# Optimization experiments

Hardware: AMD Instinct MI355X
Metric: run time of the kernel (lower is better)

Reference implementation:

```python
import jax, jax.numpy as jnp
import numpy as np

WS = 8          # window_size
DISP = WS // 2  # cyclic shift displacement
HEADS = 12
HEAD_DIM = 32
SCALE = HEAD_DIM ** -0.5


def _rel_indices():
    # indices of (x, y) for x in range(WS) for y in range(WS)
    idx = np.stack(np.meshgrid(np.arange(WS), np.arange(WS), indexing='ij'), -1).reshape(-1, 2)
    return idx[None, :, :] - idx[:, None, :] + WS - 1  # (WS^2, WS^2, 2), values in [0, 2*WS-2]


def _masks():
    ninf = -np.inf
    # upper/lower mask: blocks attention across the vertical wrap boundary
    m_ul = np.zeros((WS * WS, WS * WS), np.float32)
    m_ul[-DISP * WS:, :-DISP * WS] = ninf
    m_ul[:-DISP * WS, -DISP * WS:] = ninf
    # left/right mask: blocks attention across the horizontal wrap boundary
    m4 = np.zeros((WS, WS, WS, WS), np.float32)  # (h1, w1, h2, w2)
    m4[:, -DISP:, :, :-DISP] = ninf
    m4[:, :-DISP, :, -DISP:] = ninf
    m_lr = m4.reshape(WS * WS, WS * WS)
    return jnp.asarray(m_ul), jnp.asarray(m_lr)


def setup_inputs() -> dict:
    key = jax.random.key(0)
    k1, k2, k3, k4, k5 = jax.random.split(key, 5)
    dim = HEADS * HEAD_DIM  # 384
    return {
        'x': jax.random.normal(k1, (16, 64, 64, dim), jnp.float32),
        'w_qkv': jax.random.normal(k2, (dim, 3 * dim), jnp.float32) * 0.02,
        'pos_embedding': jax.random.normal(k3, (2 * WS - 1, 2 * WS - 1), jnp.float32),
        'w_out': jax.random.normal(k4, (dim, dim), jnp.float32) * 0.02,
        'b_out': jax.random.normal(k5, (dim,), jnp.float32) * 0.02,
    }


def reference(x, w_qkv, pos_embedding, w_out, b_out):
    b, H, W, dim = x.shape
    nw_h, nw_w = H // WS, W // WS
    # cyclic shift
    x = jnp.roll(x, (-DISP, -DISP), axis=(1, 2))
    qkv = x @ w_qkv  # (b, H, W, 3*inner)

    def to_windows(t):
        # (b, H, W, inner) -> (b, heads, nw_h*nw_w, WS*WS, head_dim)
        t = t.reshape(b, nw_h, WS, nw_w, WS, HEADS, HEAD_DIM)
        return t.transpose(0, 5, 1, 3, 2, 4, 6).reshape(b, HEADS, nw_h * nw_w, WS * WS, HEAD_DIM)

    q, k, v = [to_windows(t) for t in jnp.split(qkv, 3, axis=-1)]
    dots = jnp.einsum('bhwid,bhwjd->bhwij', q, k) * SCALE

    rel = _rel_indices()
    dots = dots + pos_embedding[rel[..., 0], rel[..., 1]]  # relative position bias

    m_ul, m_lr = _masks()
    dots = dots.at[:, :, -nw_w:].add(m_ul)            # last row of windows
    dots = dots.at[:, :, nw_w - 1::nw_w].add(m_lr)    # last column of windows

    attn = jax.nn.softmax(dots, axis=-1)
    out = jnp.einsum('bhwij,bhwjd->bhwid', attn, v)
    # windows -> image layout
    out = out.reshape(b, HEADS, nw_h, nw_w, WS, WS, HEAD_DIM)
    out = out.transpose(0, 2, 4, 3, 5, 1, 6).reshape(b, H, W, HEADS * HEAD_DIM)
    out = out @ w_out + b_out
    # cyclic back shift
    return jnp.roll(out, (DISP, DISP), axis=(1, 2))
```

## Files before the change

### kernel.cpp

```cpp
#include <hip/hip_runtime.h>
#include <stdint.h>

#define HEADS 12
#define HD 32
#define DIM 384
#define NQKV 1152
#define NPIX 4096
#define NB 16

typedef __attribute__((ext_vector_type(8))) short bf16x8;
typedef __attribute__((ext_vector_type(4))) float f32x4;

__device__ __forceinline__ unsigned short f2bf(float f) {
  uint32_t u = __builtin_bit_cast(uint32_t, f);
  u += 0x7FFF + ((u >> 16) & 1);
  return (unsigned short)(u >> 16);
}

__device__ __forceinline__ uint32_t cvtpk(float lo, float hi) {
  uint32_t r;
  asm("v_cvt_pk_bf16_f32 %0, %1, %2" : "=v"(r) : "v"(lo), "v"(hi));
  return r;
}

#define GL_LDS(gp, lp) __builtin_amdgcn_global_load_lds( \
    (const __attribute__((address_space(1))) void*)(gp),  \
    (__attribute__((address_space(3))) void*)(lp), 16, 0, 0)

#define MFMA32 __builtin_amdgcn_mfma_f32_16x16x32_bf16

__global__ void convert_w(const float* __restrict__ wqkv,
                          const float* __restrict__ wout,
                          const float* __restrict__ pos,
                          unsigned short* __restrict__ wqkvT,
                          unsigned short* __restrict__ woutT,
                          float* __restrict__ tab) {
  int bid = blockIdx.x;
  if (bid < 1728) {
    int tid = bid * 256 + threadIdx.x;
    if (tid < NQKV * DIM) {
      int n = tid / DIM, k = tid % DIM;
      wqkvT[tid] = f2bf(wqkv[(size_t)k * NQKV + n]);
    }
    if (tid < DIM * DIM) {
      int n = tid / DIM, k = tid % DIM;
      woutT[tid] = f2bf(wout[(size_t)k * DIM + n]);
    }
  } else {
    int tid = (bid - 1728) * 256 + threadIdx.x;
    int v = tid >> 12, rem = tid & 4095;
    int i = rem >> 6, j = rem & 63;
    int xi = i >> 3, yi = i & 7, xj = j >> 3, yj = j & 7;
    float val = pos[(xj - xi + 7) * 15 + (yj - yi + 7)];
    if ((v & 1) && ((i >= 32) != (j >= 32))) val = -1e30f;
    if ((v & 2) && ((yi >= 4) != (yj >= 4))) val = -1e30f;
    tab[tid] = val;
  }
}

__global__ __launch_bounds__(256, 3) void gemm_qkv(
    const float* __restrict__ x,
    const unsigned short* __restrict__ wT,
    unsigned short* __restrict__ qkv)
{
  __shared__ float lAf[128 * 64];
  __shared__ unsigned short lB[128 * 64];
  const int tid = threadIdx.x;
  const int wid = tid >> 6, lane = tid & 63;
  const int wr = wid >> 1, wc = wid & 1;
  const int lr = lane >> 4, lc = lane & 15;

  const int f = blockIdx.x;
  const int xcd = f & 7, idx = f >> 3;
  const int nt = idx % 9, mt = xcd * 64 + idx / 9;
  const int m0 = mt * 128, n0 = nt * 128;

  const int sArow = wid * 4 + (lane >> 4);
  const int sAcol = ((lane & 15) ^ sArow) * 4;
  const float* agp = x + (size_t)(m0 + sArow) * DIM + sAcol;

  const int sBrow = wid * 32 + (lane >> 3);
  const int sBcol = ((lane & 7) ^ (lane >> 3)) * 8;
  const unsigned short* bgp = wT + (size_t)(n0 + sBrow) * DIM + sBcol;

  const f32x4 z4 = {0.f, 0.f, 0.f, 0.f};
  f32x4 acc[4][4];
#pragma unroll
  for (int i = 0; i < 4; i++)
#pragma unroll
    for (int j = 0; j < 4; j++) acc[i][j] = z4;

  auto stage = [&](int t) {
#pragma unroll
    for (int i = 0; i < 8; i++)
      GL_LDS(agp + (size_t)(i * 16) * DIM + t * 64, &lAf[i * 1024 + wid * 256]);
#pragma unroll
    for (int i = 0; i < 4; i++)
      GL_LDS(bgp + (size_t)(i * 8) * DIM + t * 64, &lB[(wid * 4 + i) * 512]);
  };
  auto compute = [&]() {
    const int swb = lc & 7;
#pragma unroll
    for (int kk = 0; kk < 2; kk++) {
      bf16x8 afr[4], bfr[4];
#pragma unroll
      for (int mi = 0; mi < 4; mi++) {
        const int r = wr * 64 + mi * 16 + lc;
        const int g0 = kk * 8 + lr * 2;
        float4 a0 = *(const float4*)&lAf[r * 64 + ((g0 ^ lc) * 4)];
        float4 a1 = *(const float4*)&lAf[r * 64 + (((g0 + 1) ^ lc) * 4)];
        union { uint32_t u[4]; bf16x8 v; } up;
        up.u[0] = cvtpk(a0.x, a0.y);
        up.u[1] = cvtpk(a0.z, a0.w);
        up.u[2] = cvtpk(a1.x, a1.y);
        up.u[3] = cvtpk(a1.z, a1.w);
        afr[mi] = up.v;
      }
#pragma unroll
      for (int ni = 0; ni < 4; ni++)
        bfr[ni] = *(const bf16x8*)&lB[(wc * 64 + ni * 16 + lc) * 64 + (((kk * 4 + lr) ^ swb) * 8)];
#pragma unroll
      for (int mi = 0; mi < 4; mi++)
#pragma unroll
        for (int ni = 0; ni < 4; ni++)
          acc[mi][ni] = MFMA32(afr[mi], bfr[ni], acc[mi][ni], 0, 0, 0);
    }
  };

  for (int t = 0; t < 6; ++t) {
    stage(t);
    __syncthreads();
    compute();
    if (t < 5) __syncthreads();
  }

#pragma unroll
  for (int mi = 0; mi < 4; mi++) {
    int row = m0 + wr * 64 + mi * 16 + lr * 4;
#pragma unroll
    for (int reg = 0; reg < 4; reg++) {
      size_t rb = (size_t)(row + reg) * NQKV + n0 + wc * 64 + lc;
#pragma unroll
      for (int ni = 0; ni < 4; ni++)
        qkv[rb + ni * 16] = f2bf(acc[mi][ni][reg]);
    }
  }
}

__global__ __launch_bounds__(256) void attn_kernel(
    const unsigned short* __restrict__ qkv,
    const float* __restrict__ tab,
    unsigned short* __restrict__ Z)
{
  __shared__ unsigned short Vt[4][32 * 80];

  const int wid = threadIdx.x >> 6, lane = threadIdx.x & 63;
  const int lr = lane >> 4, lc = lane & 15;
  const int task = blockIdx.x * 4 + wid;
  const int win = task & 63;
  const int head = (task >> 6) % HEADS;
  const int b = task / (HEADS * 64);
  const int wh = win >> 3, ww = win & 7;
  const float* tv = tab + (((wh == 7) ? 1 : 0) + ((ww == 7) ? 2 : 0)) * 4096;

  auto pixof = [&](int t) {
    int hh = (wh * 8 + (t >> 3) + 4) & 63;
    int w2 = (ww * 8 + (t & 7) + 4) & 63;
    return hh * 64 + w2;
  };

  unsigned short* vt = &Vt[wid][0];
  bf16x8 qf[4], kf[4];
#pragma unroll
  for (int g = 0; g < 4; ++g) {
    int t = g * 16 + lc;
    const unsigned short* base =
        qkv + (size_t)(b * NPIX + pixof(t)) * NQKV + head * HD + lr * 8;
    qf[g] = *(const bf16x8*)(base);
    kf[g] = *(const bf16x8*)(base + DIM);
    union { bf16x8 v; unsigned short s[8]; } uv;
    uv.v = *(const bf16x8*)(base + 2 * DIM);
#pragma unroll
    for (int j = 0; j < 8; j++) {
      int row = lr * 8 + j;
      int addr = row * 80 + (((g * 2 + (lc >> 3)) ^ ((row >> 2) & 3)) << 3) + (lc & 7);
      vt[addr] = uv.s[j];
    }
  }

  const float SC = 0.17677669529663687f;
  const f32x4 z4 = {0.f, 0.f, 0.f, 0.f};
  uint32_t pf[4][2][4];
  const int srcA = (lc + 16 * (2 * (lr & 1))) << 2;
  const int srcB = srcA + 64;
  const bool hiSel = (lr >> 1) != 0;

#pragma unroll
  for (int bq = 0; bq < 4; bq++) {
    f32x4 tb[4];
#pragma unroll
    for (int a = 0; a < 4; a++)
      tb[a] = *(const f32x4*)&tv[(bq * 16 + lc) * 64 + a * 16 + lr * 4];
    f32x4 s[4];
#pragma unroll
    for (int a = 0; a < 4; a++)
      s[a] = MFMA32(kf[a], qf[bq], z4, 0, 0, 0);

    float m = -3.0e38f;
#pragma unroll
    for (int a = 0; a < 4; a++)
#pragma unroll
      for (int r = 0; r < 4; r++) {
        float val = s[a][r] * SC + tb[a][r];
        s[a][r] = val;
        m = fmaxf(m, val);
      }
    m = fmaxf(m, __shfl_xor(m, 16));
    m = fmaxf(m, __shfl_xor(m, 32));
    float sum = 0.f;
#pragma unroll
    for (int a = 0; a < 4; a++)
#pragma unroll
      for (int r = 0; r < 4; r++) {
        float p = exp2f((s[a][r] - m) * 1.44269504f);
        s[a][r] = p;
        sum += p;
      }
    sum += __shfl_xor(sum, 16);
    sum += __shfl_xor(sum, 32);
    float iv = 1.0f / sum;

    uint32_t pk[4][2];
#pragma unroll
    for (int a = 0; a < 4; a++)
#pragma unroll
      for (int w = 0; w < 2; w++)
        pk[a][w] = cvtpk(s[a][2 * w] * iv, s[a][2 * w + 1] * iv);
#pragma unroll
    for (int kk = 0; kk < 2; kk++)
#pragma unroll
      for (int wp = 0; wp < 4; wp++) {
        int sa = (wp >> 1) ? srcB : srcA;
        uint32_t lo = (uint32_t)__builtin_amdgcn_ds_bpermute(sa, (int)pk[2 * kk][wp & 1]);
        uint32_t hi = (uint32_t)__builtin_amdgcn_ds_bpermute(sa, (int)pk[2 * kk + 1][wp & 1]);
        pf[bq][kk][wp] = hiSel ? hi : lo;
      }
  }

  asm volatile("s_waitcnt lgkmcnt(0)" ::: "memory");

  f32x4 oacc[4][2];
#pragma unroll
  for (int i = 0; i < 4; i++) { oacc[i][0] = z4; oacc[i][1] = z4; }

#pragma unroll
  for (int kk = 0; kk < 2; kk++) {
    bf16x8 vfr[2];
#pragma unroll
    for (int dt = 0; dt < 2; dt++) {
      int rowd = dt * 16 + lc;
      int addr = rowd * 80 + ((((kk * 4 + lr) ^ (lc >> 2)) & 7) << 3);
      vfr[dt] = *(const bf16x8*)&vt[addr];
    }
#pragma unroll
    for (int mi = 0; mi < 4; mi++) {
      union { uint32_t u[4]; bf16x8 v; } pu;
      pu.u[0] = pf[mi][kk][0]; pu.u[1] = pf[mi][kk][1];
      pu.u[2] = pf[mi][kk][2]; pu.u[3] = pf[mi][kk][3];
#pragma unroll
      for (int dt = 0; dt < 2; dt++)
        oacc[mi][dt] = MFMA32(pu.v, vfr[dt], oacc[mi][dt], 0, 0, 0);
    }
  }

#pragma unroll
  for (int mi = 0; mi < 4; mi++) {
#pragma unroll
    for (int reg = 0; reg < 4; reg++) {
      int i = mi * 16 + lr * 4 + reg;
      size_t zb = ((size_t)b * NPIX + pixof(i)) * DIM + head * HD;
#pragma unroll
      for (int dt = 0; dt < 2; dt++)
        Z[zb + dt * 16 + lc] = f2bf(oacc[mi][dt][reg]);
    }
  }
}

__global__ __launch_bounds__(256, 4) void gemm_out(
    const unsigned short* __restrict__ Zb,
    const unsigned short* __restrict__ wT,
    const float* __restrict__ bout,
    float* __restrict__ out)
{
  __shared__ unsigned short lA[128 * 64];
  __shared__ unsigned short lB[128 * 64];
  const int tid = threadIdx.x;
  const int wid = tid >> 6, lane = tid & 63;
  const int wr = wid >> 1, wc = wid & 1;
  const int lr = lane >> 4, lc = lane & 15;

  const int f = blockIdx.x;
  const int xcd = f & 7, idx = f >> 3;
  const int nt = idx % 3, mt = xcd * 64 + idx / 3;
  const int m0 = mt * 128, n0 = nt * 128;

  const int srow = wid * 32 + (lane >> 3);
  const int scol = ((lane & 7) ^ (lane >> 3)) * 8;
  const unsigned short* agp = Zb + (size_t)(m0 + srow) * DIM + scol;
  const unsigned short* bgp = wT + (size_t)(n0 + srow) * DIM + scol;

  const f32x4 z4 = {0.f, 0.f, 0.f, 0.f};
  f32x4 acc[4][4];
#pragma unroll
  for (int i = 0; i < 4; i++)
#pragma unroll
    for (int j = 0; j < 4; j++) acc[i][j] = z4;

  auto stage = [&](int t) {
#pragma unroll
    for (int i = 0; i < 4; i++) {
      GL_LDS(agp + (size_t)(i * 8) * DIM + t * 64, &lA[(wid * 4 + i) * 512]);
      GL_LDS(bgp + (size_t)(i * 8) * DIM + t * 64, &lB[(wid * 4 + i) * 512]);
    }
  };
  auto compute = [&]() {
    const int sw = lc & 7;
#pragma unroll
    for (int kk = 0; kk < 2; kk++) {
      bf16x8 afr[4], bfr[4];
#pragma unroll
      for (int mi = 0; mi < 4; mi++)
        afr[mi] = *(const bf16x8*)&lA[(wr * 64 + mi * 16 + lc) * 64 + (((kk * 4 + lr) ^ sw) * 8)];
#pragma unroll
      for (int ni = 0; ni < 4; ni++)
        bfr[ni] = *(const bf16x8*)&lB[(wc * 64 + ni * 16 + lc) * 64 + (((kk * 4 + lr) ^ sw) * 8)];
#pragma unroll
      for (int mi = 0; mi < 4; mi++)
#pragma unroll
        for (int ni = 0; ni < 4; ni++)
          acc[mi][ni] = MFMA32(afr[mi], bfr[ni], acc[mi][ni], 0, 0, 0);
    }
  };

  for (int t = 0; t < 6; ++t) {
    stage(t);
    __syncthreads();
    compute();
    if (t < 5) __syncthreads();
  }

  float bo[4];
#pragma unroll
  for (int ni = 0; ni < 4; ni++) bo[ni] = bout[n0 + wc * 64 + ni * 16 + lc];

#pragma unroll
  for (int mi = 0; mi < 4; mi++) {
    int row = m0 + wr * 64 + mi * 16 + lr * 4;
#pragma unroll
    for (int reg = 0; reg < 4; reg++) {
      size_t rb = (size_t)(row + reg) * DIM + n0 + wc * 64 + lc;
#pragma unroll
      for (int ni = 0; ni < 4; ni++)
        out[rb + ni * 16] = acc[mi][ni][reg] + bo[ni];
    }
  }
}

extern "C" void kernel_launch(void* const* d_in, const int* in_sizes, int n_in,
                              void* d_out, int out_size, void* d_ws, size_t ws_size,
                              hipStream_t stream) {
  const float* x    = (const float*)d_in[0];
  const float* wqkv = (const float*)d_in[1];
  const float* pos  = (const float*)d_in[2];
  const float* wout = (const float*)d_in[3];
  const float* bout = (const float*)d_in[4];
  float* out = (float*)d_out;

  char* ws = (char*)d_ws;
  unsigned short* wqkvT = (unsigned short*)ws;
  unsigned short* woutT = (unsigned short*)(ws + 884736);
  unsigned short* qkv   = (unsigned short*)(ws + 1179648);
  unsigned short* Zb    = (unsigned short*)(ws + 1179648 + 150994944);
  float* tab = out;

  convert_w<<<1792, 256, 0, stream>>>(wqkv, wout, pos, wqkvT, woutT, tab);
  gemm_qkv<<<4608, 256, 0, stream>>>(x, wqkvT, qkv);
  attn_kernel<<<3072, 256, 0, stream>>>(qkv, tab, Zb);
  gemm_out<<<1536, 256, 0, stream>>>(Zb, woutT, bout, out);
}
```

Measured before the change: 213.0 us.

## Convert QKV GEMM A-tile to bf16 at staging instead of per-MFMA read

The A operand (fp32 x) was loaded into LDS as fp32 via direct global-to-LDS copies and converted to bf16 on every fragment read. It is now loaded into registers, converted once, and written to LDS as swizzled bf16. This halves the A-tile LDS footprint and removes repeated conversions, and launch bounds rise to 4 blocks per CU. In exchange, A staging now goes through registers with synchronous global loads, which may expose latency and raise register pressure.

```diff
diff --git a/kernel.cpp b/kernel.cpp
--- a/kernel.cpp
+++ b/kernel.cpp
@@ -58,12 +58,12 @@
   }
 }
 
-__global__ __launch_bounds__(256, 3) void gemm_qkv(
+__global__ __launch_bounds__(256, 4) void gemm_qkv(
     const float* __restrict__ x,
     const unsigned short* __restrict__ wT,
     unsigned short* __restrict__ qkv)
 {
-  __shared__ float lAf[128 * 64];
+  __shared__ unsigned short lA[128 * 64];
   __shared__ unsigned short lB[128 * 64];
   const int tid = threadIdx.x;
   const int wid = tid >> 6, lane = tid & 63;
@@ -75,9 +75,11 @@
   const int nt = idx % 9, mt = xcd * 64 + idx / 9;
   const int m0 = mt * 128, n0 = nt * 128;
 
-  const int sArow = wid * 4 + (lane >> 4);
-  const int sAcol = ((lane & 15) ^ sArow) * 4;
-  const float* agp = x + (size_t)(m0 + sArow) * DIM + sAcol;
+  const int ar = tid >> 1;
+  const int ag = (tid & 1) * 4;
+  const float* axp = x + (size_t)(m0 + ar) * DIM + ag * 8;
+  unsigned short* awp = &lA[ar * 64];
+  const int akey = ar & 7;
 
   const int sBrow = wid * 32 + (lane >> 3);
   const int sBcol = ((lane & 7) ^ (lane >> 3)) * 8;
@@ -92,33 +94,31 @@
 
   auto stage = [&](int t) {
 #pragma unroll
-    for (int i = 0; i < 8; i++)
-      GL_LDS(agp + (size_t)(i * 16) * DIM + t * 64, &lAf[i * 1024 + wid * 256]);
-#pragma unroll
     for (int i = 0; i < 4; i++)
       GL_LDS(bgp + (size_t)(i * 8) * DIM + t * 64, &lB[(wid * 4 + i) * 512]);
+#pragma unroll
+    for (int q = 0; q < 4; ++q) {
+      float4 f0 = *(const float4*)(axp + t * 64 + q * 8);
+      float4 f1 = *(const float4*)(axp + t * 64 + q * 8 + 4);
+      union { uint32_t u[4]; bf16x8 v; } up;
+      up.u[0] = cvtpk(f0.x, f0.y);
+      up.u[1] = cvtpk(f0.z, f0.w);
+      up.u[2] = cvtpk(f1.x, f1.y);
+      up.u[3] = cvtpk(f1.z, f1.w);
+      *(bf16x8*)&awp[((ag + q) ^ akey) * 8] = up.v;
+    }
   };
   auto compute = [&]() {
-    const int swb = lc & 7;
+    const int sw = lc & 7;
 #pragma unroll
     for (int kk = 0; kk < 2; kk++) {
       bf16x8 afr[4], bfr[4];
 #pragma unroll
-      for (int mi = 0; mi < 4; mi++) {
-        const int r = wr * 64 + mi * 16 + lc;
-        const int g0 = kk * 8 + lr * 2;
-        float4 a0 = *(const float4*)&lAf[r * 64 + ((g0 ^ lc) * 4)];
-        float4 a1 = *(const float4*)&lAf[r * 64 + (((g0 + 1) ^ lc) * 4)];
-        union { uint32_t u[4]; bf16x8 v; } up;
-        up.u[0] = cvtpk(a0.x, a0.y);
-        up.u[1] = cvtpk(a0.z, a0.w);
-        up.u[2] = cvtpk(a1.x, a1.y);
-        up.u[3] = cvtpk(a1.z, a1.w);
-        afr[mi] = up.v;
-      }
+      for (int mi = 0; mi < 4; mi++)
+        afr[mi] = *(const bf16x8*)&lA[(wr * 64 + mi * 16 + lc) * 64 + (((kk * 4 + lr) ^ sw) * 8)];
 #pragma unroll
       for (int ni = 0; ni < 4; ni++)
-        bfr[ni] = *(const bf16x8*)&lB[(wc * 64 + ni * 16 + lc) * 64 + (((kk * 4 + lr) ^ swb) * 8)];
+        bfr[ni] = *(const bf16x8*)&lB[(wc * 64 + ni * 16 + lc) * 64 + (((kk * 4 + lr) ^ sw) * 8)];
 #pragma unroll
       for (int mi = 0; mi < 4; mi++)
 #pragma unroll
```

After: 333.5 us. 1.57x slower.
